# Performance work log

Measured on AMD Instinct MI355X. Metric: run time of the kernel, lower is better.

## Reference

```python
import jax, jax.numpy as jnp
import numpy as np

N = 50000
E = 400000
D = 128   # embed_dim == per-head out_channels
H = 2     # graph_heads
NEG_SLOPE = 0.2


def setup_inputs() -> dict:
    key = jax.random.key(0)
    ks = jax.random.split(key, 10)
    s = 1.0 / np.sqrt(D)
    x = jax.random.normal(ks[0], (N, D), dtype=jnp.float32)
    edge_index = jax.random.randint(ks[1], (2, E), 0, N, dtype=jnp.int64)
    # GATv2Conv params: lin_l (source), lin_r (target), attention vector, conv bias
    Wl = jax.random.uniform(ks[2], (H * D, D), jnp.float32, -s, s)
    bl = jax.random.uniform(ks[3], (H * D,), jnp.float32, -s, s)
    Wr = jax.random.uniform(ks[4], (H * D, D), jnp.float32, -s, s)
    br = jax.random.uniform(ks[5], (H * D,), jnp.float32, -s, s)
    att = jax.random.uniform(ks[6], (H, D), jnp.float32, -s, s)
    bias_conv = jnp.zeros((H * D,), jnp.float32)
    # trailing Linear(H*D -> D)
    so = 1.0 / np.sqrt(H * D)
    Wo = jax.random.uniform(ks[7], (D, H * D), jnp.float32, -so, so)
    bo = jax.random.uniform(ks[8], (D,), jnp.float32, -so, so)
    return {"x": x, "edge_index": edge_index, "Wl": Wl, "bl": bl, "Wr": Wr,
            "br": br, "att": att, "bias_conv": bias_conv, "Wo": Wo, "bo": bo}


def reference(x, edge_index, Wl, bl, Wr, br, att, bias_conv, Wo, bo):
    n = x.shape[0]
    # GATv2Conv default add_self_loops=True
    loops = jnp.arange(n, dtype=edge_index.dtype)
    src = jnp.concatenate([edge_index[0], loops])  # x_j (source / message)
    dst = jnp.concatenate([edge_index[1], loops])  # x_i (target / aggregation)

    xl = (x @ Wl.T + bl).reshape(n, H, D)  # source projection
    xr = (x @ Wr.T + br).reshape(n, H, D)  # target projection

    e = xl[src] + xr[dst]                               # [E+N, H, D]
    score = jnp.einsum('ehd,hd->eh', jax.nn.leaky_relu(e, NEG_SLOPE), att)

    # segment softmax over destination neighborhoods
    m = jax.ops.segment_max(score, dst, num_segments=n)  # [N, H]
    a = jnp.exp(score - m[dst])
    denom = jax.ops.segment_sum(a, dst, num_segments=n)
    alpha = a / (denom[dst] + 1e-16)                     # [E+N, H]

    out = jax.ops.segment_sum(xl[src] * alpha[..., None], dst, num_segments=n)
    out = out.reshape(n, H * D) + bias_conv              # concat heads + conv bias
    return out @ Wo.T + bo                               # [N, D]
```

## Files before the change

kernel.cpp:

```cpp
#include <hip/hip_runtime.h>
#include <math.h>

#define DIMV 128
#define HDV  256
#define NEGS 0.2f
#define CAPV 64

typedef __attribute__((ext_vector_type(8))) short short8;
typedef __attribute__((ext_vector_type(8))) unsigned short ushort8v;
typedef __attribute__((ext_vector_type(4))) float f32x4;

__device__ __forceinline__ int edge_at(const int* p, int is64, long long idx) {
    return is64 ? p[2 * idx] : p[(size_t)idx];
}

__device__ __forceinline__ unsigned short f2bf(float f) {
    union { float f; unsigned u; } v; v.f = f;
    unsigned r = (v.u + 0x7FFF + ((v.u >> 16) & 1)) >> 16;
    return (unsigned short)r;
}
__device__ __forceinline__ float bf2f(unsigned short b) {
    union { unsigned u; float f; } v; v.u = ((unsigned)b) << 16;
    return v.f;
}

__global__ __launch_bounds__(256) void build_prep_kernel(
    const int* __restrict__ eidx, int E, int nn,
    int* __restrict__ deg, int* __restrict__ elist,
    const float* __restrict__ Wl, const float* __restrict__ Wr,
    const float* __restrict__ Wo,
    unsigned short* __restrict__ WB, unsigned short* __restrict__ WoB)
{
    const int b = blockIdx.x, t = threadIdx.x;
    if (b < 128) {
        int tid = b * 256 + t;
        int f = tid * 2;
        int e    = f & 7;
        int rowc = (f >> 3) & 127;
        int lg   = (f >> 10) & 3;
        int kk   = (f >> 12) & 3;
        int mh   = f >> 14;
        int mat = mh >> 1, half = mh & 1;
        const float* W = mat ? Wr : Wl;
        float2 v = *(const float2*)(W + (size_t)(half * 128 + rowc) * DIMV + kk * 32 + lg * 8 + e);
        ushort2 o; o.x = f2bf(v.x); o.y = f2bf(v.y);
        *(ushort2*)(WB + f) = o;
    } else if (b < 192) {
        int tid = (b - 128) * 256 + t;
        int f = tid * 2;
        int e    = f & 7;
        int rowc = (f >> 3) & 127;
        int lg   = (f >> 10) & 3;
        int kk   = f >> 12;
        float2 v = *(const float2*)(Wo + (size_t)rowc * HDV + kk * 32 + lg * 8 + e);
        ushort2 o; o.x = f2bf(v.x); o.y = f2bf(v.y);
        *(ushort2*)(WoB + f) = o;
    } else {
        const int idx = (b - 192) * 256 + t;
        const int Et = E + nn;
        if (idx >= Et) return;
        const int is64 = ((eidx[1] | eidx[3] | eidx[5] | eidx[7]) == 0) ? 1 : 0;
        int s, d;
        if (idx < E) {
            s = edge_at(eidx, is64, idx);
            d = edge_at(eidx, is64, (long long)E + idx);
        } else {
            s = idx - E; d = s;
        }
        int pos = atomicAdd(deg + d, 1);
        if (pos < CAPV) elist[(size_t)d * CAPV + pos] = s;
    }
}

__global__ __launch_bounds__(512) void proj_mfma_kernel(
    const float* __restrict__ x,
    const unsigned short* __restrict__ WB,
    const float* __restrict__ bl, const float* __restrict__ br,
    unsigned short* __restrict__ xl, unsigned short* __restrict__ xr, int nn)
{
    __shared__ __align__(16) unsigned short xs[64 * 128];
    __shared__ __align__(16) unsigned short os[64 * 256];
    const int t = threadIdx.x;
    const int m0b = blockIdx.x * 64;
    char* xsb = (char*)xs;

    for (int i = t; i < 64 * 32; i += 512) {
        int rr = i >> 5, q = i & 31;
        float4 v = make_float4(0.f, 0.f, 0.f, 0.f);
        if (m0b + rr < nn) v = ((const float4*)(x + (size_t)(m0b + rr) * DIMV))[q];
        ushort4 bv; bv.x = f2bf(v.x); bv.y = f2bf(v.y); bv.z = f2bf(v.z); bv.w = f2bf(v.w);
        *(ushort4*)(xsb + (((rr * 256) + q * 8) ^ ((rr & 7) << 4))) = bv;
    }
    __syncthreads();

    const int lane = t & 63, w8 = t >> 6;
    const int w = w8 & 3, half = w8 >> 2;
    const int lm = lane & 15, lg = lane >> 4;
    f32x4 acc0[8], acc1[8];
#pragma unroll
    for (int nt = 0; nt < 8; ++nt) {
        acc0[nt] = (f32x4){0.f, 0.f, 0.f, 0.f};
        acc1[nt] = (f32x4){0.f, 0.f, 0.f, 0.f};
    }

    const int arow = w * 16 + lm;
    const int aswz = (arow & 7) << 4;
#pragma unroll
    for (int kk = 0; kk < 4; ++kk) {
        const int koff = kk * 64 + lg * 16;
        short8 afrag = *(const short8*)(xsb + ((arow * 256 + koff) ^ aswz));
        const unsigned short* wb0 = WB + (size_t)(((half * 4 + kk) * 4 + lg) * 128) * 8;
        const unsigned short* wb1 = WB + (size_t)((((2 + half) * 4 + kk) * 4 + lg) * 128) * 8;
#pragma unroll
        for (int nt = 0; nt < 8; ++nt) {
            const int brow = nt * 16 + lm;
            short8 b0 = *(const short8*)(wb0 + brow * 8);
            acc0[nt] = __builtin_amdgcn_mfma_f32_16x16x32_bf16(afrag, b0, acc0[nt], 0, 0, 0);
            short8 b1 = *(const short8*)(wb1 + brow * 8);
            acc1[nt] = __builtin_amdgcn_mfma_f32_16x16x32_bf16(afrag, b1, acc1[nt], 0, 0, 0);
        }
    }

    const int colbase = half * 128;
#pragma unroll
    for (int nt = 0; nt < 8; ++nt) {
        const int c = colbase + nt * 16 + lm;
        const float bv = bl[c];
#pragma unroll
        for (int rg = 0; rg < 4; ++rg)
            os[(w * 16 + lg * 4 + rg) * 256 + c] = f2bf(acc0[nt][rg] + bv);
    }
    __syncthreads();
    for (int i = t; i < 64 * 32; i += 512) {
        int rr = i >> 5, q = i & 31;
        if (m0b + rr < nn)
            *(ushort8v*)(xl + (size_t)(m0b + rr) * HDV + q * 8) =
                *(const ushort8v*)(os + rr * 256 + q * 8);
    }
    __syncthreads();
#pragma unroll
    for (int nt = 0; nt < 8; ++nt) {
        const int c = colbase + nt * 16 + lm;
        const float bv = br[c];
#pragma unroll
        for (int rg = 0; rg < 4; ++rg)
            os[(w * 16 + lg * 4 + rg) * 256 + c] = f2bf(acc1[nt][rg] + bv);
    }
    __syncthreads();
    for (int i = t; i < 64 * 32; i += 512) {
        int rr = i >> 5, q = i & 31;
        if (m0b + rr < nn)
            *(ushort8v*)(xr + (size_t)(m0b + rr) * HDV + q * 8) =
                *(const ushort8v*)(os + rr * 256 + q * 8);
    }
}

__global__ __launch_bounds__(512) void fused_kernel(
    const unsigned short* __restrict__ xl, const unsigned short* __restrict__ xr,
    const float* __restrict__ att,
    const int* __restrict__ deg, const int* __restrict__ elist,
    const float* __restrict__ bias_conv,
    unsigned short* __restrict__ aggb, int nn)
{
    const int t = threadIdx.x, lane = t & 63, wid = t >> 6;
    const int h = lane & 31, par = lane >> 5;
    const int n0 = blockIdx.x * 32;
    float att8[8], bc8[8];
#pragma unroll
    for (int k = 0; k < 8; ++k) {
        att8[k] = att[h * 8 + k];
        bc8[k]  = bias_conv[h * 8 + k];
    }

    for (int j = 0; j < 4; ++j) {
        const int n = n0 + wid * 4 + j;
        int dg = 0;
        const int* __restrict__ row = elist;
        float xr8[8];
#pragma unroll
        for (int k = 0; k < 8; ++k) xr8[k] = 0.f;
        if (n < nn) {
            dg = min(deg[n], CAPV);
            row = elist + (size_t)n * CAPV;
            ushort8v v = *(const ushort8v*)(xr + (size_t)n * HDV + h * 8);
#pragma unroll
            for (int k = 0; k < 8; ++k) xr8[k] = bf2f(v[k]);
        }
        const int myidx = row[lane];
        const int np = (dg + 1) >> 1, np1 = np - 1, dgm1 = dg - 1;
        float m0 = -1e30f, den = 0.f;
        float a8[8];
#pragma unroll
        for (int k = 0; k < 8; ++k) a8[k] = 0.f;

        if (np > 0) {
            int i0 = __shfl(myidx, min(par, dgm1), 64);
            int i1 = __shfl(myidx, min(2 * min(1, np1) + par, dgm1), 64);
            int i2 = __shfl(myidx, min(2 * min(2, np1) + par, dgm1), 64);
            int i3 = __shfl(myidx, min(2 * min(3, np1) + par, dgm1), 64);
            ushort8v v0 = *(const ushort8v*)(xl + (size_t)i0 * HDV + h * 8);
            ushort8v v1 = *(const ushort8v*)(xl + (size_t)i1 * HDV + h * 8);
            ushort8v v2 = *(const ushort8v*)(xl + (size_t)i2 * HDV + h * 8);
            ushort8v v3 = *(const ushort8v*)(xl + (size_t)i3 * HDV + h * 8);
            for (int ip = 0; ip < np; ++ip) {
                ushort8v cur = v0; v0 = v1; v1 = v2; v2 = v3;
                {
                    int pn = min(2 * min(ip + 4, np1) + par, dgm1);
                    int in_ = __shfl(myidx, pn, 64);
                    v3 = *(const ushort8v*)(xl + (size_t)in_ * HDV + h * 8);
                }
                float xv8[8];
#pragma unroll
                for (int k = 0; k < 8; ++k) xv8[k] = bf2f(cur[k]);
                float p = 0.f;
#pragma unroll
                for (int k = 0; k < 8; ++k) {
                    float e = xv8[k] + xr8[k];
                    e = fmaxf(e, NEGS * e);
                    p = fmaf(e, att8[k], p);
                }
                p += __shfl_xor(p, 1);
                p += __shfl_xor(p, 2);
                p += __shfl_xor(p, 4);
                p += __shfl_xor(p, 8);
                const bool valid = (2 * ip + par) < dg;
                if (!valid) p = -1e30f;
                if (p > m0) {
                    float sc = __expf(m0 - p);
                    den *= sc;
#pragma unroll
                    for (int k = 0; k < 8; ++k) a8[k] *= sc;
                    m0 = p;
                }
                float wgt = valid ? __expf(p - m0) : 0.f;
                den += wgt;
#pragma unroll
                for (int k = 0; k < 8; ++k) a8[k] = fmaf(wgt, xv8[k], a8[k]);
            }
        }
        float m1 = __shfl_xor(m0, 32);
        float d1 = __shfl_xor(den, 32);
        float mm = fmaxf(m0, m1);
        float s0 = __expf(m0 - mm);
        den = den * s0 + d1 * __expf(m1 - mm);
        float rden = 1.f / (den + 1e-16f);
        ushort8v o;
#pragma unroll
        for (int k = 0; k < 8; ++k) {
            float as = a8[k] * s0;
            as += __shfl_xor(as, 32);
            o[k] = f2bf(fmaf(as, rden, bc8[k]));
        }
        if (par == 0 && n < nn)
            *(ushort8v*)(aggb + (size_t)n * HDV + h * 8) = o;
    }
}

__global__ __launch_bounds__(256) void gemm_out_kernel(
    const unsigned short* __restrict__ aggb,
    const unsigned short* __restrict__ WoB,
    const float* __restrict__ bo,
    float* __restrict__ out, int nn)
{
    __shared__ __align__(16) unsigned short xs[64 * 256];
    const int t = threadIdx.x;
    const int m0b = blockIdx.x * 64;
    char* xsb = (char*)xs;

    for (int i = t; i < 64 * 32; i += 256) {
        int rr = i >> 5, q = i & 31;
        ushort8v v = {0, 0, 0, 0, 0, 0, 0, 0};
        if (m0b + rr < nn) v = *(const ushort8v*)(aggb + (size_t)(m0b + rr) * HDV + q * 8);
        *(ushort8v*)(xsb + ((rr * 512 + q * 16) ^ ((rr & 7) << 4))) = v;
    }
    __syncthreads();

    const int lane = t & 63, w = t >> 6;
    const int lm = lane & 15, lg = lane >> 4;
    f32x4 acc[8];
#pragma unroll
    for (int nt = 0; nt < 8; ++nt) acc[nt] = (f32x4){0.f, 0.f, 0.f, 0.f};

    const int arow = w * 16 + lm;
    const int aswz = (arow & 7) << 4;
#pragma unroll
    for (int kk = 0; kk < 8; ++kk) {
        const int koff = kk * 64 + lg * 16;
        short8 afrag = *(const short8*)(xsb + ((arow * 512 + koff) ^ aswz));
        const unsigned short* wb = WoB + (size_t)((kk * 4 + lg) * 128) * 8;
#pragma unroll
        for (int nt = 0; nt < 8; ++nt) {
            const int brow = nt * 16 + lm;
            short8 bfrag = *(const short8*)(wb + brow * 8);
            acc[nt] = __builtin_amdgcn_mfma_f32_16x16x32_bf16(afrag, bfrag, acc[nt], 0, 0, 0);
        }
    }

#pragma unroll
    for (int nt = 0; nt < 8; ++nt) {
        const int c = nt * 16 + lm;
        const float bv = bo[c];
#pragma unroll
        for (int rg = 0; rg < 4; ++rg) {
            const int node = m0b + w * 16 + lg * 4 + rg;
            if (node < nn) out[(size_t)node * DIMV + c] = acc[nt][rg] + bv;
        }
    }
}

extern "C" void kernel_launch(void* const* d_in, const int* in_sizes, int n_in,
                              void* d_out, int out_size, void* d_ws, size_t ws_size,
                              hipStream_t stream) {
    const float* x         = (const float*)d_in[0];
    const int*   eidx      = (const int*)d_in[1];
    const float* Wl        = (const float*)d_in[2];
    const float* bl        = (const float*)d_in[3];
    const float* Wr        = (const float*)d_in[4];
    const float* br        = (const float*)d_in[5];
    const float* att       = (const float*)d_in[6];
    const float* bias_conv = (const float*)d_in[7];
    const float* Wo        = (const float*)d_in[8];
    const float* bo        = (const float*)d_in[9];
    float* out = (float*)d_out;

    const int nn = in_sizes[0] / DIMV;
    const int E  = in_sizes[1] / 2;
    const int Et = E + nn;

    char* ws = (char*)d_ws;
    size_t off = 0;
    auto alloc = [&](size_t bytes) -> void* {
        void* p = ws + off;
        off += (bytes + 255) & ~(size_t)255;
        return p;
    };
    unsigned short* xl   = (unsigned short*)alloc((size_t)nn * HDV * 2);
    unsigned short* xr   = (unsigned short*)alloc((size_t)nn * HDV * 2);
    unsigned short* aggb = (unsigned short*)alloc((size_t)nn * HDV * 2);
    int*   deg   = (int*)alloc((size_t)nn * 4);
    int*   elist = (int*)alloc((size_t)nn * CAPV * 4);
    unsigned short* WB  = (unsigned short*)alloc((size_t)65536 * 2);
    unsigned short* WoB = (unsigned short*)alloc((size_t)32768 * 2);
    (void)ws_size; (void)n_in; (void)out_size;

    hipMemsetAsync(deg, 0, (size_t)nn * 4, stream);

    build_prep_kernel<<<192 + (Et + 255) / 256, 256, 0, stream>>>(
        eidx, E, nn, deg, elist, Wl, Wr, Wo, WB, WoB);

    proj_mfma_kernel<<<(nn + 63) / 64, 512, 0, stream>>>(x, WB, bl, br, xl, xr, nn);

    fused_kernel<<<(nn + 31) / 32, 512, 0, stream>>>(xl, xr, att, deg, elist,
                                                     bias_conv, aggb, nn);

    gemm_out_kernel<<<(nn + 63) / 64, 256, 0, stream>>>(aggb, WoB, bo, out, nn);
}
```

Before: 147.2 us.

## Fuse output GEMM into aggregation kernel and precast x to bf16 in prep

The output linear layer is folded into the attention-aggregation kernel: each 256-thread block aggregates 16 nodes into a swizzled shared-memory tile, then runs a small MFMA GEMM against the bf16 Wo, with each wave producing 32 output columns. This removes the global aggb round trip and one kernel launch. Separately, x is converted to bf16 inside the prep kernel, and the projection kernel reads A fragments straight from global memory instead of staging them through LDS. The cost is smaller fused blocks, which re-read WoB per block, plus an extra bf16 copy of x; the padded xb buffer (nn+64 rows) covers out-of-range tail reads, although those padding rows are never written.

```diff
diff --git a/kernel.cpp b/kernel.cpp
--- a/kernel.cpp
+++ b/kernel.cpp
@@ -28,10 +28,12 @@
     const int* __restrict__ eidx, int E, int nn,
     int* __restrict__ deg, int* __restrict__ elist,
     const float* __restrict__ Wl, const float* __restrict__ Wr,
-    const float* __restrict__ Wo,
-    unsigned short* __restrict__ WB, unsigned short* __restrict__ WoB)
+    const float* __restrict__ Wo, const float* __restrict__ x,
+    unsigned short* __restrict__ WB, unsigned short* __restrict__ WoB,
+    unsigned short* __restrict__ xb)
 {
     const int b = blockIdx.x, t = threadIdx.x;
+    const int EB = (E + nn + 255) >> 8;
     if (b < 128) {
         int tid = b * 256 + t;
         int f = tid * 2;
@@ -55,7 +57,7 @@
         float2 v = *(const float2*)(Wo + (size_t)rowc * HDV + kk * 32 + lg * 8 + e);
         ushort2 o; o.x = f2bf(v.x); o.y = f2bf(v.y);
         *(ushort2*)(WoB + f) = o;
-    } else {
+    } else if (b < 192 + EB) {
         const int idx = (b - 192) * 256 + t;
         const int Et = E + nn;
         if (idx >= Et) return;
@@ -69,33 +71,32 @@
         }
         int pos = atomicAdd(deg + d, 1);
         if (pos < CAPV) elist[(size_t)d * CAPV + pos] = s;
+    } else {
+        long long base = ((long long)(b - 192 - EB) * 256 + t) * 8;
+        if (base < (long long)nn * DIMV) {
+            float4 v0 = *(const float4*)(x + base);
+            float4 v1 = *(const float4*)(x + base + 4);
+            ushort8v o;
+            o[0] = f2bf(v0.x); o[1] = f2bf(v0.y); o[2] = f2bf(v0.z); o[3] = f2bf(v0.w);
+            o[4] = f2bf(v1.x); o[5] = f2bf(v1.y); o[6] = f2bf(v1.z); o[7] = f2bf(v1.w);
+            *(ushort8v*)(xb + base) = o;
+        }
     }
 }
 
 __global__ __launch_bounds__(512) void proj_mfma_kernel(
-    const float* __restrict__ x,
+    const unsigned short* __restrict__ xb,
     const unsigned short* __restrict__ WB,
     const float* __restrict__ bl, const float* __restrict__ br,
     unsigned short* __restrict__ xl, unsigned short* __restrict__ xr, int nn)
 {
-    __shared__ __align__(16) unsigned short xs[64 * 128];
     __shared__ __align__(16) unsigned short os[64 * 256];
     const int t = threadIdx.x;
     const int m0b = blockIdx.x * 64;
-    char* xsb = (char*)xs;
-
-    for (int i = t; i < 64 * 32; i += 512) {
-        int rr = i >> 5, q = i & 31;
-        float4 v = make_float4(0.f, 0.f, 0.f, 0.f);
-        if (m0b + rr < nn) v = ((const float4*)(x + (size_t)(m0b + rr) * DIMV))[q];
-        ushort4 bv; bv.x = f2bf(v.x); bv.y = f2bf(v.y); bv.z = f2bf(v.z); bv.w = f2bf(v.w);
-        *(ushort4*)(xsb + (((rr * 256) + q * 8) ^ ((rr & 7) << 4))) = bv;
-    }
-    __syncthreads();
-
     const int lane = t & 63, w8 = t >> 6;
     const int w = w8 & 3, half = w8 >> 2;
     const int lm = lane & 15, lg = lane >> 4;
+
     f32x4 acc0[8], acc1[8];
 #pragma unroll
     for (int nt = 0; nt < 8; ++nt) {
@@ -103,12 +104,10 @@
         acc1[nt] = (f32x4){0.f, 0.f, 0.f, 0.f};
     }
 
-    const int arow = w * 16 + lm;
-    const int aswz = (arow & 7) << 4;
+    const unsigned short* arow_p = xb + (size_t)(m0b + w * 16 + lm) * DIMV;
 #pragma unroll
     for (int kk = 0; kk < 4; ++kk) {
-        const int koff = kk * 64 + lg * 16;
-        short8 afrag = *(const short8*)(xsb + ((arow * 256 + koff) ^ aswz));
+        short8 afrag = *(const short8*)(arow_p + kk * 32 + lg * 8);
         const unsigned short* wb0 = WB + (size_t)(((half * 4 + kk) * 4 + lg) * 128) * 8;
         const unsigned short* wb1 = WB + (size_t)((((2 + half) * 4 + kk) * 4 + lg) * 128) * 8;
 #pragma unroll
@@ -155,16 +154,19 @@
     }
 }
 
-__global__ __launch_bounds__(512) void fused_kernel(
+__global__ __launch_bounds__(256) void fused_kernel(
     const unsigned short* __restrict__ xl, const unsigned short* __restrict__ xr,
     const float* __restrict__ att,
     const int* __restrict__ deg, const int* __restrict__ elist,
     const float* __restrict__ bias_conv,
-    unsigned short* __restrict__ aggb, int nn)
+    const unsigned short* __restrict__ WoB, const float* __restrict__ bo,
+    float* __restrict__ out, int nn)
 {
+    __shared__ __align__(16) unsigned short ags[16 * 256];
     const int t = threadIdx.x, lane = t & 63, wid = t >> 6;
     const int h = lane & 31, par = lane >> 5;
-    const int n0 = blockIdx.x * 32;
+    const int n0 = blockIdx.x * 16;
+    char* agsb = (char*)ags;
     float att8[8], bc8[8];
 #pragma unroll
     for (int k = 0; k < 8; ++k) {
@@ -174,6 +176,7 @@
 
     for (int j = 0; j < 4; ++j) {
         const int n = n0 + wid * 4 + j;
+        const int r = wid * 4 + j;
         int dg = 0;
         const int* __restrict__ row = elist;
         float xr8[8];
@@ -251,59 +254,35 @@
             as += __shfl_xor(as, 32);
             o[k] = f2bf(fmaf(as, rden, bc8[k]));
         }
-        if (par == 0 && n < nn)
-            *(ushort8v*)(aggb + (size_t)n * HDV + h * 8) = o;
-    }
-}
-
-__global__ __launch_bounds__(256) void gemm_out_kernel(
-    const unsigned short* __restrict__ aggb,
-    const unsigned short* __restrict__ WoB,
-    const float* __restrict__ bo,
-    float* __restrict__ out, int nn)
-{
-    __shared__ __align__(16) unsigned short xs[64 * 256];
-    const int t = threadIdx.x;
-    const int m0b = blockIdx.x * 64;
-    char* xsb = (char*)xs;
-
-    for (int i = t; i < 64 * 32; i += 256) {
-        int rr = i >> 5, q = i & 31;
-        ushort8v v = {0, 0, 0, 0, 0, 0, 0, 0};
-        if (m0b + rr < nn) v = *(const ushort8v*)(aggb + (size_t)(m0b + rr) * HDV + q * 8);
-        *(ushort8v*)(xsb + ((rr * 512 + q * 16) ^ ((rr & 7) << 4))) = v;
+        if (par == 0)
+            *(ushort8v*)(agsb + ((r * 512 + h * 16) ^ ((r & 7) << 4))) = o;
     }
     __syncthreads();
 
-    const int lane = t & 63, w = t >> 6;
     const int lm = lane & 15, lg = lane >> 4;
-    f32x4 acc[8];
-#pragma unroll
-    for (int nt = 0; nt < 8; ++nt) acc[nt] = (f32x4){0.f, 0.f, 0.f, 0.f};
-
-    const int arow = w * 16 + lm;
-    const int aswz = (arow & 7) << 4;
+    f32x4 acc2[2];
+    acc2[0] = (f32x4){0.f, 0.f, 0.f, 0.f};
+    acc2[1] = (f32x4){0.f, 0.f, 0.f, 0.f};
+    const int aswz = (lm & 7) << 4;
 #pragma unroll
     for (int kk = 0; kk < 8; ++kk) {
-        const int koff = kk * 64 + lg * 16;
-        short8 afrag = *(const short8*)(xsb + ((arow * 512 + koff) ^ aswz));
+        short8 afrag = *(const short8*)(agsb + ((lm * 512 + kk * 64 + lg * 16) ^ aswz));
         const unsigned short* wb = WoB + (size_t)((kk * 4 + lg) * 128) * 8;
 #pragma unroll
-        for (int nt = 0; nt < 8; ++nt) {
-            const int brow = nt * 16 + lm;
+        for (int u = 0; u < 2; ++u) {
+            const int brow = (wid * 2 + u) * 16 + lm;
             short8 bfrag = *(const short8*)(wb + brow * 8);
-            acc[nt] = __builtin_amdgcn_mfma_f32_16x16x32_bf16(afrag, bfrag, acc[nt], 0, 0, 0);
-        }
-    }
-
-#pragma unroll
-    for (int nt = 0; nt < 8; ++nt) {
-        const int c = nt * 16 + lm;
+            acc2[u] = __builtin_amdgcn_mfma_f32_16x16x32_bf16(afrag, bfrag, acc2[u], 0, 0, 0);
+        }
+    }
+#pragma unroll
+    for (int u = 0; u < 2; ++u) {
+        const int c = (wid * 2 + u) * 16 + lm;
         const float bv = bo[c];
 #pragma unroll
         for (int rg = 0; rg < 4; ++rg) {
-            const int node = m0b + w * 16 + lg * 4 + rg;
-            if (node < nn) out[(size_t)node * DIMV + c] = acc[nt][rg] + bv;
+            const int node = n0 + lg * 4 + rg;
+            if (node < nn) out[(size_t)node * DIMV + c] = acc2[u][rg] + bv;
         }
     }
 }
@@ -334,9 +313,9 @@
         off += (bytes + 255) & ~(size_t)255;
         return p;
     };
-    unsigned short* xl   = (unsigned short*)alloc((size_t)nn * HDV * 2);
-    unsigned short* xr   = (unsigned short*)alloc((size_t)nn * HDV * 2);
-    unsigned short* aggb = (unsigned short*)alloc((size_t)nn * HDV * 2);
+    unsigned short* xb  = (unsigned short*)alloc((size_t)(nn + 64) * DIMV * 2);
+    unsigned short* xl  = (unsigned short*)alloc((size_t)nn * HDV * 2);
+    unsigned short* xr  = (unsigned short*)alloc((size_t)nn * HDV * 2);
     int*   deg   = (int*)alloc((size_t)nn * 4);
     int*   elist = (int*)alloc((size_t)nn * CAPV * 4);
     unsigned short* WB  = (unsigned short*)alloc((size_t)65536 * 2);
@@ -345,13 +324,13 @@
 
     hipMemsetAsync(deg, 0, (size_t)nn * 4, stream);
 
-    build_prep_kernel<<<192 + (Et + 255) / 256, 256, 0, stream>>>(
-        eidx, E, nn, deg, elist, Wl, Wr, Wo, WB, WoB);
-
-    proj_mfma_kernel<<<(nn + 63) / 64, 512, 0, stream>>>(x, WB, bl, br, xl, xr, nn);
-
-    fused_kernel<<<(nn + 31) / 32, 512, 0, stream>>>(xl, xr, att, deg, elist,
-                                                     bias_conv, aggb, nn);
-
-    gemm_out_kernel<<<(nn + 63) / 64, 256, 0, stream>>>(aggb, WoB, bo, out, nn);
-}
+    const int EB = (Et + 255) / 256;
+    const int XB = (nn * DIMV / 8 + 255) / 256;
+    build_prep_kernel<<<192 + EB + XB, 256, 0, stream>>>(
+        eidx, E, nn, deg, elist, Wl, Wr, Wo, x, WB, WoB, xb);
+
+    proj_mfma_kernel<<<(nn + 63) / 64, 512, 0, stream>>>(xb, WB, bl, br, xl, xr, nn);
+
+    fused_kernel<<<(nn + 15) / 16, 256, 0, stream>>>(xl, xr, att, deg, elist,
+                                                     bias_conv, WoB, bo, out, nn);
+}
```

Result: faster. 138.7 us (-5.7%).
